# Kernel optimization log

Hardware: AMD Instinct MI355X
Metric: run time of the kernel (lower is better)

Reference implementation:

```python
import math
import jax, jax.numpy as jnp
import numpy as np

B, S, G, CMAX, T = 128, 256, 8, 6, 32
E, NH, L, Z = 64, 4, 2, 3
DFF = 4 * E


def _conv1d(x, w, b, pad):
    # x: [N, C, T], w: [O, I, K] -> [N, O, T]
    y = jax.lax.conv_general_dilated(x, w, (1,), [(pad, pad)], dimension_numbers=('NCH', 'OIH', 'NCH'))
    return y + b[None, :, None]


def _layernorm(x, g, b, eps=1e-5):
    m = jnp.mean(x, -1, keepdims=True)
    v = jnp.mean((x - m) ** 2, -1, keepdims=True)
    return (x - m) * jax.lax.rsqrt(v + eps) * g + b


def _pos_encoding(seq_len, dim):
    pos = jnp.arange(seq_len, dtype=jnp.float32)[:, None]
    div = jnp.exp(jnp.arange(0, dim, 2, dtype=jnp.float32) * (-math.log(10000.0) / dim))
    pe = jnp.zeros((seq_len, dim), dtype=jnp.float32)
    pe = pe.at[:, 0::2].set(jnp.sin(pos * div)).at[:, 1::2].set(jnp.cos(pos * div))
    return pe


def setup_inputs() -> dict:
    key = jax.random.key(0)
    ks = iter(jax.random.split(key, 48))
    def nrm(shape, s=0.05):
        return (jax.random.normal(next(ks), shape) * s).astype(jnp.float32)
    inp = {}
    inp['waveforms'] = jax.random.normal(next(ks), (B, S, CMAX, T), dtype=jnp.float32)
    inp['shank_ids'] = jax.random.randint(next(ks), (B, S), 0, G)
    lengths = jax.random.randint(next(ks), (B,), S // 2, S + 1)
    inp['mask'] = jnp.arange(S)[None, :] >= lengths[:, None]  # True = padded
    inp['conv1_w'] = nrm((G, 32, CMAX, 5), 0.1)
    inp['conv1_b'] = jnp.zeros((G, 32), jnp.float32)
    inp['conv2_w'] = nrm((G, E, 32, 3), 0.1)
    inp['conv2_b'] = jnp.zeros((G, E), jnp.float32)
    inp['shank_emb'] = nrm((G, E), 0.02)
    inp['in_proj_w'] = nrm((L, 3 * E, E))
    inp['in_proj_b'] = jnp.zeros((L, 3 * E), jnp.float32)
    inp['out_proj_w'] = nrm((L, E, E))
    inp['out_proj_b'] = jnp.zeros((L, E), jnp.float32)
    inp['ln1_g'] = jnp.ones((L, E), jnp.float32)
    inp['ln1_b'] = jnp.zeros((L, E), jnp.float32)
    inp['ff1_w'] = nrm((L, DFF, E))
    inp['ff1_b'] = jnp.zeros((L, DFF), jnp.float32)
    inp['ff2_w'] = nrm((L, E, DFF))
    inp['ff2_b'] = jnp.zeros((L, E), jnp.float32)
    inp['ln2_g'] = jnp.ones((L, E), jnp.float32)
    inp['ln2_b'] = jnp.zeros((L, E), jnp.float32)
    inp['cls_w1'] = nrm((E, E)); inp['cls_b1'] = jnp.zeros((E,), jnp.float32)
    inp['cls_w2'] = nrm((Z, E)); inp['cls_b2'] = jnp.zeros((Z,), jnp.float32)
    inp['mu_w1'] = nrm((Z, E, E)); inp['mu_b1'] = jnp.zeros((Z, E), jnp.float32)
    inp['mu_w2'] = nrm((Z, 2, E)); inp['mu_b2'] = jnp.zeros((Z, 2), jnp.float32)
    inp['ls_w1'] = nrm((Z, E, E)); inp['ls_b1'] = jnp.zeros((Z, E), jnp.float32)
    inp['ls_w2'] = nrm((Z, 2, E)); inp['ls_b2'] = jnp.zeros((Z, 2), jnp.float32)
    inp['d_w1'] = nrm((E, E)); inp['d_b1'] = jnp.zeros((E,), jnp.float32)
    inp['d_w2'] = nrm((1, E)); inp['d_b2'] = jnp.zeros((1,), jnp.float32)
    return inp


def reference(waveforms, shank_ids, mask, conv1_w, conv1_b, conv2_w, conv2_b, shank_emb,
              in_proj_w, in_proj_b, out_proj_w, out_proj_b, ln1_g, ln1_b,
              ff1_w, ff1_b, ff2_w, ff2_b, ln2_g, ln2_b,
              cls_w1, cls_b1, cls_w2, cls_b2, mu_w1, mu_b1, mu_w2, mu_b2,
              ls_w1, ls_b1, ls_w2, ls_b2, d_w1, d_b1, d_w2, d_b2):
    b, s, c, t = waveforms.shape
    e = shank_emb.shape[1]
    g = shank_emb.shape[0]
    x = waveforms.reshape(b * s, c, t)
    # per-shank conv encoders (MoE-style dispatch); loop over fixed small expert set
    embs = []
    for i in range(g):
        h1 = jax.nn.relu(_conv1d(x, conv1_w[i], conv1_b[i], 2))   # [N,32,T]
        h2 = jax.nn.relu(_conv1d(h1, conv2_w[i], conv2_b[i], 1))  # [N,E,T]
        embs.append(h2.mean(-1))                                  # AdaptiveAvgPool1d(1)
    emb_all = jnp.stack(embs, axis=1)                             # [N,G,E]
    sid = shank_ids.reshape(-1)
    emb = jnp.take_along_axis(emb_all, sid[:, None, None], axis=1)[:, 0]  # [N,E]
    active = (~mask).reshape(-1)
    emb = jnp.where(active[:, None], emb, 0.0).reshape(b, s, e)   # masked slots stay zero
    emb = emb + shank_emb[shank_ids] + _pos_encoding(s, e)[None]
    # post-norm transformer encoder, relu FFN, eval mode (dropout off)
    dh = e // NH
    key_bias = jnp.where(mask, -1e9, 0.0).astype(emb.dtype)[:, None, None, :]  # [B,1,1,S]
    h = emb
    for l in range(in_proj_w.shape[0]):
        qkv = h @ in_proj_w[l].T + in_proj_b[l]
        q, k, v = jnp.split(qkv, 3, axis=-1)
        q = q.reshape(b, s, NH, dh)
        k = k.reshape(b, s, NH, dh)
        v = v.reshape(b, s, NH, dh)
        scores = jnp.einsum('bqhd,bkhd->bhqk', q, k) / math.sqrt(dh) + key_bias
        attn = jax.nn.softmax(scores, axis=-1)
        o = jnp.einsum('bhqk,bkhd->bqhd', attn, v).reshape(b, s, e)
        o = o @ out_proj_w[l].T + out_proj_b[l]
        h = _layernorm(h + o, ln1_g[l], ln1_b[l])
        ff = jax.nn.relu(h @ ff1_w[l].T + ff1_b[l]) @ ff2_w[l].T + ff2_b[l]
        h = _layernorm(h + ff, ln2_g[l], ln2_b[l])
    am = active.reshape(b, s, 1).astype(h.dtype)
    pooled = (h * am).sum(1) / (am.sum(1) + 1e-8)                 # masked mean pool [B,E]
    cls_logits = jax.nn.relu(pooled @ cls_w1.T + cls_b1) @ cls_w2.T + cls_b2
    hz = jax.nn.relu(jnp.einsum('be,zfe->zbf', pooled, mu_w1) + mu_b1[:, None])
    mus = jnp.einsum('zbf,zof->bzo', hz, mu_w2) + mu_b2[None]     # [B,Z,2]
    hs = jax.nn.relu(jnp.einsum('be,zfe->zbf', pooled, ls_w1) + ls_b1[:, None])
    sigmas = jnp.exp(jnp.einsum('zbf,zof->bzo', hs, ls_w2) + ls_b2[None])  # [B,Z,2]
    d_pred = jax.nn.sigmoid(jax.nn.relu(pooled @ d_w1.T + d_b1) @ d_w2.T + d_b2)
    return jnp.concatenate([cls_logits, mus.reshape(b, -1), sigmas.reshape(b, -1), d_pred], axis=-1)
```

## Files before the change

### kernel.cpp

```cpp
#include <hip/hip_runtime.h>
#include <math.h>


typedef short bf16x8 __attribute__((ext_vector_type(8)));
typedef float f32x4 __attribute__((ext_vector_type(4)));

__device__ __forceinline__ unsigned short f2bf(float f) {
  unsigned u = __float_as_uint(f);
  u += 0x7fffu + ((u >> 16) & 1u);
  return (unsigned short)(u >> 16);
}

__device__ __forceinline__ bf16x8 ldfrag(const unsigned short* p) {
  return *reinterpret_cast<const bf16x8*>(p);
}

__device__ __forceinline__ bool is_masked(const void* mask_, int flag, int idx) {
  return flag ? (((const unsigned char*)mask_)[idx] != 0)
              : (((const int*)mask_)[idx] != 0);
}

__global__ void detect_mask_kernel(const unsigned int* __restrict__ mw,
                                   int* __restrict__ flag, int* __restrict__ counts,
                                   int* __restrict__ lens) {
  __shared__ int sh;
  if (threadIdx.x == 0) sh = 0;
  __syncthreads();
  int bad = 0;
  for (int i = threadIdx.x; i < 8192; i += 256)
    if (mw[i] > 1u) bad = 1;
  if (bad) atomicOr(&sh, 1);
  if (threadIdx.x < 8) counts[threadIdx.x] = 0;
  if (threadIdx.x < 128) lens[threadIdx.x] = 0;
  __syncthreads();
  if (threadIdx.x == 0) *flag = sh;
}

__global__ __launch_bounds__(256) void bin_kernel(
    const int* __restrict__ sid, const void* __restrict__ mask_,
    const int* __restrict__ flagp, int* __restrict__ counts,
    int* __restrict__ lens, int* __restrict__ idxbuf) {
  __shared__ int lcnt[8];
  __shared__ int lbase[8];
  int b = blockIdx.x, tid = threadIdx.x;
  int n = b * 256 + tid;
  int flag = *flagp;
  bool act = !is_masked(mask_, flag, n);
  int g = act ? sid[n] : 0;
  if (tid < 8) lcnt[tid] = 0;
  __syncthreads();
  int pos = 0;
  if (act) pos = atomicAdd(&lcnt[g], 1);
  __syncthreads();
  if (tid < 8) lbase[tid] = atomicAdd(&counts[tid], lcnt[tid]);
  if (tid == 0)
    lens[b] = lcnt[0] + lcnt[1] + lcnt[2] + lcnt[3] +
              lcnt[4] + lcnt[5] + lcnt[6] + lcnt[7];
  __syncthreads();
  if (act) idxbuf[g * 32768 + lbase[g] + pos] = n;
}

__global__ __launch_bounds__(256) void init_emb_kernel(
    const int* __restrict__ sid, const float* __restrict__ shank_emb,
    float* __restrict__ hout) {
  int i = blockIdx.x * 256 + threadIdx.x;
  int n = i >> 6, e = i & 63, s = n & 255;
  int g = sid[n];
  float div = __expf(-(float)(e & ~1) * (9.21034037f / 64.f));
  float angle = (float)s * div;
  float pe = (e & 1) ? cosf(angle) : sinf(angle);
  hout[i] = shank_emb[g * 64 + e] + pe;
}

__global__ __launch_bounds__(256) void conv_mfma_kernel(
    const int* __restrict__ idxbuf, const int* __restrict__ counts,
    const float* __restrict__ wav,
    const float* __restrict__ w1_, const float* __restrict__ b1_,
    const float* __restrict__ w2_, const float* __restrict__ b2_,
    const float* __restrict__ shank_emb, float* __restrict__ hout) {
  __shared__ __align__(16) unsigned short w1f[5][32][8];
  __shared__ __align__(16) unsigned short w2f[3][64][40];
  __shared__ float b1s[32];
  __shared__ float b2s[64];
  __shared__ __align__(16) unsigned short xw[4][36][8];
  __shared__ __align__(16) unsigned short h1w[4][34][40];
  int g = blockIdx.x & 7, bib = blockIdx.x >> 3;
  int tid = threadIdx.x;
  int wvx = tid >> 6, lane = tid & 63, quad = lane >> 4, l15 = lane & 15;
  for (int i = tid; i < 1280; i += 256) {
    int k = i >> 8, rest = i & 255, oc = rest >> 3, ic = rest & 7;
    w1f[k][oc][ic] = (ic < 6) ? f2bf(w1_[g * 960 + oc * 30 + ic * 5 + k]) : 0;
  }
  for (int i = tid; i < 7680; i += 256) {
    int k = i / 2560, rest = i % 2560, e = rest / 40, ic = rest % 40;
    w2f[k][e][ic] = (ic < 32) ? f2bf(w2_[g * 6144 + e * 96 + ic * 3 + k]) : 0;
  }
  if (tid < 32) b1s[tid] = b1_[g * 32 + tid];
  if (tid < 64) b2s[tid] = b2_[g * 64 + tid];
  {
    unsigned int* xz = (unsigned int*)&xw[wvx][0][0];
    for (int i = lane; i < 144; i += 64) xz[i] = 0;
    unsigned int* hz0 = (unsigned int*)&h1w[wvx][0][0];
    unsigned int* hz1 = (unsigned int*)&h1w[wvx][33][0];
    if (lane < 20) hz0[lane] = 0;
    else if (lane < 40) hz1[lane - 20] = 0;
  }
  __syncthreads();
  bf16x8 zf = {0, 0, 0, 0, 0, 0, 0, 0};
  bf16x8 bf1[2], bf1k4[2], bf2[3][4];
#pragma unroll
  for (int nt = 0; nt < 2; nt++) {
    bf1[nt] = ldfrag(&w1f[quad][nt * 16 + l15][0]);
    bf1k4[nt] = (quad == 0) ? ldfrag(&w1f[4][nt * 16 + l15][0]) : zf;
  }
#pragma unroll
  for (int k = 0; k < 3; k++)
#pragma unroll
    for (int nt = 0; nt < 4; nt++)
      bf2[k][nt] = ldfrag(&w2f[k][nt * 16 + l15][quad * 8]);
  float b1v0 = b1s[l15], b1v1 = b1s[16 + l15];
  float shank = shank_emb[g * 64 + lane];
  float dive = __expf(-(float)(lane & ~1) * (9.21034037f / 64.f));
  int cnt = counts[g];
  int wvg = bib * 4 + wvx;
  int ic_w = lane >> 3, t0_w = (lane & 7) * 4;
  for (int ti = wvg; ti < cnt; ti += 512) {
    int n = idxbuf[g * 32768 + ti];
    float4 v = make_float4(0.f, 0.f, 0.f, 0.f);
    if (lane < 48) v = *(const float4*)&wav[n * 192 + lane * 4];
    if (lane < 48) {
      xw[wvx][t0_w + 2][ic_w] = f2bf(v.x);
      xw[wvx][t0_w + 3][ic_w] = f2bf(v.y);
      xw[wvx][t0_w + 4][ic_w] = f2bf(v.z);
      xw[wvx][t0_w + 5][ic_w] = f2bf(v.w);
    }
    f32x4 c1[2][2];
#pragma unroll
    for (int mt = 0; mt < 2; mt++) {
      c1[mt][0] = (f32x4){b1v0, b1v0, b1v0, b1v0};
      c1[mt][1] = (f32x4){b1v1, b1v1, b1v1, b1v1};
    }
#pragma unroll
    for (int mt = 0; mt < 2; mt++) {
      bf16x8 afm = ldfrag(&xw[wvx][mt * 16 + l15 + quad][0]);
      bf16x8 af4 = (quad == 0) ? ldfrag(&xw[wvx][mt * 16 + l15 + 4][0]) : zf;
#pragma unroll
      for (int nt = 0; nt < 2; nt++) {
        c1[mt][nt] = __builtin_amdgcn_mfma_f32_16x16x32_bf16(afm, bf1[nt], c1[mt][nt], 0, 0, 0);
        c1[mt][nt] = __builtin_amdgcn_mfma_f32_16x16x32_bf16(af4, bf1k4[nt], c1[mt][nt], 0, 0, 0);
      }
    }
#pragma unroll
    for (int mt = 0; mt < 2; mt++)
#pragma unroll
      for (int nt = 0; nt < 2; nt++)
#pragma unroll
        for (int r = 0; r < 4; r++) {
          int t = mt * 16 + quad * 4 + r;
          h1w[wvx][t + 1][nt * 16 + l15] = f2bf(fmaxf(c1[mt][nt][r], 0.f));
        }
    f32x4 c2[2][4];
#pragma unroll
    for (int mt = 0; mt < 2; mt++)
#pragma unroll
      for (int nt = 0; nt < 4; nt++) {
        float bv = b2s[nt * 16 + l15];
        c2[mt][nt] = (f32x4){bv, bv, bv, bv};
      }
#pragma unroll
    for (int k = 0; k < 3; k++)
#pragma unroll
      for (int mt = 0; mt < 2; mt++) {
        bf16x8 af = ldfrag(&h1w[wvx][mt * 16 + l15 + k][quad * 8]);
#pragma unroll
        for (int nt = 0; nt < 4; nt++)
          c2[mt][nt] = __builtin_amdgcn_mfma_f32_16x16x32_bf16(af, bf2[k][nt], c2[mt][nt], 0, 0, 0);
      }
    float sums[4];
#pragma unroll
    for (int nt = 0; nt < 4; nt++) {
      float s = 0.f;
#pragma unroll
      for (int mt = 0; mt < 2; mt++)
#pragma unroll
        for (int r = 0; r < 4; r++) s += fmaxf(c2[mt][nt][r], 0.f);
      s += __shfl_xor(s, 16);
      s += __shfl_xor(s, 32);
      sums[nt] = s;
    }
    float t0 = __shfl(sums[0], l15);
    float t1 = __shfl(sums[1], l15);
    float t2 = __shfl(sums[2], l15);
    float t3 = __shfl(sums[3], l15);
    float val = (quad == 0) ? t0 : (quad == 1) ? t1 : (quad == 2) ? t2 : t3;
    float angle = (float)(n & 255) * dive;
    float pe = (lane & 1) ? cosf(angle) : sinf(angle);
    hout[(size_t)n * 64 + lane] = val * (1.f / 32.f) + shank + pe;
  }
}

__global__ __launch_bounds__(256) void attn_fused_kernel(
    const float* __restrict__ H, const float* __restrict__ Wqkv,
    const float* __restrict__ bqkv, const int* __restrict__ lens,
    float* __restrict__ o) {
  __shared__ __align__(16) unsigned short un[18432];
  __shared__ __align__(16) unsigned short wqs[16][72];
  __shared__ __align__(16) unsigned short wks[16][72];
  __shared__ __align__(16) unsigned short wvs[16][72];
  __shared__ __align__(16) unsigned short qs[256][24];
  __shared__ __align__(16) unsigned short kst[256][24];
  __shared__ __align__(16) unsigned short vT[16][264];
  __shared__ float bqs[16], bks[16], bvs[16];
  unsigned short (*hs)[72] = (unsigned short(*)[72])un;
  unsigned short (*pw)[16][264] = (unsigned short(*)[16][264])un;
  int bh = blockIdx.x;
  int b_ = bh >> 2, hd = bh & 3;
  int tid = threadIdx.x;
  int wvx = tid >> 6, lane = tid & 63, quad = lane >> 4, l15 = lane & 15;
  int len = lens[b_];
  const float* hb = H + (size_t)b_ * 256 * 64;
  for (int i = tid; i < 4096; i += 256) {
    int r = i >> 4, c4 = (i & 15) << 2;
    float4 v = *(const float4*)&hb[r * 64 + c4];
    short4 t;
    t.x = (short)f2bf(v.x); t.y = (short)f2bf(v.y);
    t.z = (short)f2bf(v.z); t.w = (short)f2bf(v.w);
    *(short4*)&hs[r][c4] = t;
  }
  for (int i = tid; i < 768; i += 256) {
    int r = i >> 4, c4 = (i & 15) << 2;
    int which = r >> 4, rr = r & 15;
    float4 v = *(const float4*)&Wqkv[(size_t)(which * 64 + hd * 16 + rr) * 64 + c4];
    float sc = (which == 0) ? 0.25f : 1.f;
    short4 t;
    t.x = (short)f2bf(v.x * sc); t.y = (short)f2bf(v.y * sc);
    t.z = (short)f2bf(v.z * sc); t.w = (short)f2bf(v.w * sc);
    unsigned short (*dst)[72] = (which == 0) ? wqs : (which == 1) ? wks : wvs;
    *(short4*)&dst[rr][c4] = t;
  }
  if (tid < 16) {
    bqs[tid] = 0.25f * bqkv[hd * 16 + tid];
    bks[tid] = bqkv[64 + hd * 16 + tid];
    bvs[tid] = bqkv[128 + hd * 16 + tid];
  }
  __syncthreads();
#pragma unroll
  for (int t4 = 0; t4 < 4; t4++) {
    int tile = wvx * 4 + t4;
    float bq = bqs[l15], bk = bks[l15];
    f32x4 aq = (f32x4){bq, bq, bq, bq};
    f32x4 ak = (f32x4){bk, bk, bk, bk};
    f32x4 av = (f32x4){bvs[quad * 4 + 0], bvs[quad * 4 + 1],
                       bvs[quad * 4 + 2], bvs[quad * 4 + 3]};
#pragma unroll
    for (int ks = 0; ks < 64; ks += 32) {
      bf16x8 af = ldfrag(&hs[tile * 16 + l15][ks + quad * 8]);
      aq = __builtin_amdgcn_mfma_f32_16x16x32_bf16(af, ldfrag(&wqs[l15][ks + quad * 8]), aq, 0, 0, 0);
      ak = __builtin_amdgcn_mfma_f32_16x16x32_bf16(af, ldfrag(&wks[l15][ks + quad * 8]), ak, 0, 0, 0);
      av = __builtin_amdgcn_mfma_f32_16x16x32_bf16(ldfrag(&wvs[l15][ks + quad * 8]), af, av, 0, 0, 0);
    }
#pragma unroll
    for (int r = 0; r < 4; r++) {
      qs[tile * 16 + quad * 4 + r][l15] = f2bf(aq[r]);
      kst[tile * 16 + quad * 4 + r][l15] = f2bf(ak[r]);
      vT[quad * 4 + r][tile * 16 + l15] = f2bf(av[r]);
    }
  }
  __syncthreads();
  bf16x8 zf = {0, 0, 0, 0, 0, 0, 0, 0};
  f32x4 zero = {0.f, 0.f, 0.f, 0.f};
#pragma unroll 1
  for (int j = 0; j < 4; j++) {
    int qt = wvx * 4 + j;
    bf16x8 bq = (quad < 2) ? ldfrag(&qs[qt * 16 + l15][quad * 8]) : zf;
    f32x4 s[16];
#pragma unroll
    for (int t = 0; t < 16; t++) {
      bf16x8 ak = (quad < 2) ? ldfrag(&kst[t * 16 + l15][quad * 8]) : zf;
      s[t] = __builtin_amdgcn_mfma_f32_16x16x32_bf16(ak, bq, zero, 0, 0, 0);
    }
    float mx = -1e30f;
#pragma unroll
    for (int t = 0; t < 16; t++)
#pragma unroll
      for (int r = 0; r < 4; r++) {
        int key = t * 16 + quad * 4 + r;
        float v = (key < len) ? s[t][r] : -1e30f;
        s[t][r] = v;
        mx = fmaxf(mx, v);
      }
    mx = fmaxf(mx, __shfl_xor(mx, 16));
    mx = fmaxf(mx, __shfl_xor(mx, 32));
    float sum = 0.f;
#pragma unroll
    for (int t = 0; t < 16; t++)
#pragma unroll
      for (int r = 0; r < 4; r++) {
        float p = __expf(s[t][r] - mx);
        s[t][r] = p;
        sum += p;
      }
    sum += __shfl_xor(sum, 16);
    sum += __shfl_xor(sum, 32);
#pragma unroll
    for (int t = 0; t < 16; t++) {
      short4 pp;
      pp.x = (short)f2bf(s[t][0]); pp.y = (short)f2bf(s[t][1]);
      pp.z = (short)f2bf(s[t][2]); pp.w = (short)f2bf(s[t][3]);
      *(short4*)&pw[wvx][l15][t * 16 + quad * 4] = pp;
    }
    f32x4 acc = zero;
#pragma unroll
    for (int c = 0; c < 8; c++) {
      bf16x8 avv = ldfrag(&vT[l15][c * 32 + quad * 8]);
      bf16x8 bp = ldfrag(&pw[wvx][l15][c * 32 + quad * 8]);
      acc = __builtin_amdgcn_mfma_f32_16x16x32_bf16(avv, bp, acc, 0, 0, 0);
    }
    float inv = 1.f / sum;
    float4 w;
    w.x = acc[0] * inv; w.y = acc[1] * inv;
    w.z = acc[2] * inv; w.w = acc[3] * inv;
    *(float4*)&o[(size_t)(b_ * 256 + qt * 16 + l15) * 64 + hd * 16 + quad * 4] = w;
  }
}

__global__ __launch_bounds__(256) void fused_rl_kernel(
    const float* __restrict__ obuf, float* __restrict__ H,
    const float* __restrict__ Wout, const float* __restrict__ bout,
    const float* __restrict__ ln1g, const float* __restrict__ ln1b,
    const float* __restrict__ Wff1, const float* __restrict__ bff1,
    const float* __restrict__ Wff2, const float* __restrict__ bff2,
    const float* __restrict__ ln2g, const float* __restrict__ ln2b) {
  __shared__ __align__(16) unsigned short Ao[64][72];
  __shared__ __align__(16) unsigned short Wo[64][72];
  __shared__ __align__(16) unsigned short W1s[256][72];
  __shared__ __align__(16) unsigned short W2s[64][264];
  __shared__ __align__(16) unsigned short h1b[64][72];
  __shared__ __align__(16) unsigned short ffa[64][264];
  __shared__ float h1f[64][68];
  int m0 = blockIdx.x * 64;
  int tid = threadIdx.x;
  int wvx = tid >> 6, lane = tid & 63, quad = lane >> 4, l15 = lane & 15;
  for (int i = tid; i < 1024; i += 256) {
    int r = i >> 4, c4 = (i & 15) << 2;
    float4 av = *(const float4*)&obuf[(size_t)(m0 + r) * 64 + c4];
    short4 t;
    t.x = (short)f2bf(av.x); t.y = (short)f2bf(av.y);
    t.z = (short)f2bf(av.z); t.w = (short)f2bf(av.w);
    *(short4*)&Ao[r][c4] = t;
    float4 wv4 = *(const float4*)&Wout[(size_t)r * 64 + c4];
    short4 u;
    u.x = (short)f2bf(wv4.x); u.y = (short)f2bf(wv4.y);
    u.z = (short)f2bf(wv4.z); u.w = (short)f2bf(wv4.w);
    *(short4*)&Wo[r][c4] = u;
  }
  for (int i = tid; i < 4096; i += 256) {
    int r = i >> 4, c4 = (i & 15) << 2;
    float4 wv4 = *(const float4*)&Wff1[(size_t)r * 64 + c4];
    short4 u;
    u.x = (short)f2bf(wv4.x); u.y = (short)f2bf(wv4.y);
    u.z = (short)f2bf(wv4.z); u.w = (short)f2bf(wv4.w);
    *(short4*)&W1s[r][c4] = u;
  }
  for (int i = tid; i < 4096; i += 256) {
    int r = i >> 6, c4 = (i & 63) << 2;
    float4 wv4 = *(const float4*)&Wff2[(size_t)r * 256 + c4];
    short4 u;
    u.x = (short)f2bf(wv4.x); u.y = (short)f2bf(wv4.y);
    u.z = (short)f2bf(wv4.z); u.w = (short)f2bf(wv4.w);
    *(short4*)&W2s[r][c4] = u;
  }
  __syncthreads();
  int lr = wvx * 16 + quad * 4;
  f32x4 acc[4];
#pragma unroll
  for (int nt = 0; nt < 4; nt++) {
    float b = bout[nt * 16 + l15];
    acc[nt] = (f32x4){b, b, b, b};
  }
#pragma unroll
  for (int ks = 0; ks < 64; ks += 32) {
    bf16x8 af = ldfrag(&Ao[wvx * 16 + l15][ks + quad * 8]);
#pragma unroll
    for (int nt = 0; nt < 4; nt++) {
      bf16x8 bfr = ldfrag(&Wo[nt * 16 + l15][ks + quad * 8]);
      acc[nt] = __builtin_amdgcn_mfma_f32_16x16x32_bf16(af, bfr, acc[nt], 0, 0, 0);
    }
  }
#pragma unroll
  for (int r = 0; r < 4; r++) {
    float rv[4];
    float s = 0.f;
#pragma unroll
    for (int nt = 0; nt < 4; nt++) {
      float v = acc[nt][r] + H[(size_t)(m0 + lr + r) * 64 + nt * 16 + l15];
      rv[nt] = v; s += v;
    }
    s += __shfl_xor(s, 1); s += __shfl_xor(s, 2);
    s += __shfl_xor(s, 4); s += __shfl_xor(s, 8);
    float mean = s * (1.f / 64.f);
    float vsum = 0.f;
#pragma unroll
    for (int nt = 0; nt < 4; nt++) { rv[nt] -= mean; vsum += rv[nt] * rv[nt]; }
    vsum += __shfl_xor(vsum, 1); vsum += __shfl_xor(vsum, 2);
    vsum += __shfl_xor(vsum, 4); vsum += __shfl_xor(vsum, 8);
    float inv = rsqrtf(vsum * (1.f / 64.f) + 1e-5f);
#pragma unroll
    for (int nt = 0; nt < 4; nt++) {
      int col = nt * 16 + l15;
      float hv = rv[nt] * inv * ln1g[col] + ln1b[col];
      h1f[lr + r][col] = hv;
      h1b[lr + r][col] = f2bf(hv);
    }
  }
  f32x4 a2[16];
#pragma unroll
  for (int nt = 0; nt < 16; nt++) {
    float b = bff1[nt * 16 + l15];
    a2[nt] = (f32x4){b, b, b, b};
  }
#pragma unroll
  for (int ks = 0; ks < 64; ks += 32) {
    bf16x8 af = ldfrag(&h1b[wvx * 16 + l15][ks + quad * 8]);
#pragma unroll
    for (int nt = 0; nt < 16; nt++) {
      bf16x8 bfr = ldfrag(&W1s[nt * 16 + l15][ks + quad * 8]);
      a2[nt] = __builtin_amdgcn_mfma_f32_16x16x32_bf16(af, bfr, a2[nt], 0, 0, 0);
    }
  }
#pragma unroll
  for (int nt = 0; nt < 16; nt++)
#pragma unroll
    for (int r = 0; r < 4; r++)
      ffa[lr + r][nt * 16 + l15] = f2bf(fmaxf(a2[nt][r], 0.f));
#pragma unroll
  for (int nt = 0; nt < 4; nt++) {
    float b = bff2[nt * 16 + l15];
    acc[nt] = (f32x4){b, b, b, b};
  }
#pragma unroll
  for (int ks = 0; ks < 256; ks += 32) {
    bf16x8 af = ldfrag(&ffa[wvx * 16 + l15][ks + quad * 8]);
#pragma unroll
    for (int nt = 0; nt < 4; nt++) {
      bf16x8 bfr = ldfrag(&W2s[nt * 16 + l15][ks + quad * 8]);
      acc[nt] = __builtin_amdgcn_mfma_f32_16x16x32_bf16(af, bfr, acc[nt], 0, 0, 0);
    }
  }
#pragma unroll
  for (int r = 0; r < 4; r++) {
    float rv[4];
    float s = 0.f;
#pragma unroll
    for (int nt = 0; nt < 4; nt++) {
      float v = acc[nt][r] + h1f[lr + r][nt * 16 + l15];
      rv[nt] = v; s += v;
    }
    s += __shfl_xor(s, 1); s += __shfl_xor(s, 2);
    s += __shfl_xor(s, 4); s += __shfl_xor(s, 8);
    float mean = s * (1.f / 64.f);
    float vsum = 0.f;
#pragma unroll
    for (int nt = 0; nt < 4; nt++) { rv[nt] -= mean; vsum += rv[nt] * rv[nt]; }
    vsum += __shfl_xor(vsum, 1); vsum += __shfl_xor(vsum, 2);
    vsum += __shfl_xor(vsum, 4); vsum += __shfl_xor(vsum, 8);
    float inv = rsqrtf(vsum * (1.f / 64.f) + 1e-5f);
#pragma unroll
    for (int nt = 0; nt < 4; nt++) {
      int col = nt * 16 + l15;
      H[(size_t)(m0 + lr + r) * 64 + col] = rv[nt] * inv * ln2g[col] + ln2b[col];
    }
  }
}

__global__ __launch_bounds__(256) void pool_heads_kernel(
    const float* __restrict__ h, const int* __restrict__ lens,
    const float* __restrict__ cls_w1, const float* __restrict__ cls_b1,
    const float* __restrict__ cls_w2, const float* __restrict__ cls_b2,
    const float* __restrict__ mu_w1, const float* __restrict__ mu_b1,
    const float* __restrict__ mu_w2, const float* __restrict__ mu_b2,
    const float* __restrict__ ls_w1, const float* __restrict__ ls_b1,
    const float* __restrict__ ls_w2, const float* __restrict__ ls_b2,
    const float* __restrict__ d_w1, const float* __restrict__ d_b1,
    const float* __restrict__ d_w2, const float* __restrict__ d_b2,
    float* __restrict__ out) {
  __shared__ float ps[4][64];
  __shared__ float p[64];
  __shared__ float t1[64];
  int b = blockIdx.x, tid = threadIdx.x;
  int e = tid & 63, sp = tid >> 6;
  int len = lens[b];
  {
    float sum = 0.f;
    int send = min(sp * 64 + 64, len);
    for (int s = sp * 64; s < send; s++) sum += h[(size_t)(b * 256 + s) * 64 + e];
    ps[sp][e] = sum;
  }
  __syncthreads();
  if (sp == 0)
    p[e] = (ps[0][e] + ps[1][e] + ps[2][e] + ps[3][e]) / ((float)len + 1e-8f);
  __syncthreads();
  if (tid < 64) {
    float a = cls_b1[tid];
    for (int j = 0; j < 64; j++) a += p[j] * cls_w1[tid * 64 + j];
    t1[tid] = fmaxf(a, 0.f);
  }
  __syncthreads();
  if (tid < 3) {
    float a2 = cls_b2[tid];
    for (int j = 0; j < 64; j++) a2 += t1[j] * cls_w2[tid * 64 + j];
    out[b * 16 + tid] = a2;
  }
  for (int z = 0; z < 3; z++) {
    __syncthreads();
    if (tid < 64) {
      float a = mu_b1[z * 64 + tid];
      for (int j = 0; j < 64; j++) a += p[j] * mu_w1[(z * 64 + tid) * 64 + j];
      t1[tid] = fmaxf(a, 0.f);
    }
    __syncthreads();
    if (tid < 2) {
      float a2 = mu_b2[z * 2 + tid];
      for (int j = 0; j < 64; j++) a2 += t1[j] * mu_w2[(z * 2 + tid) * 64 + j];
      out[b * 16 + 3 + z * 2 + tid] = a2;
    }
    __syncthreads();
    if (tid < 64) {
      float a = ls_b1[z * 64 + tid];
      for (int j = 0; j < 64; j++) a += p[j] * ls_w1[(z * 64 + tid) * 64 + j];
      t1[tid] = fmaxf(a, 0.f);
    }
    __syncthreads();
    if (tid < 2) {
      float a2 = ls_b2[z * 2 + tid];
      for (int j = 0; j < 64; j++) a2 += t1[j] * ls_w2[(z * 2 + tid) * 64 + j];
      out[b * 16 + 9 + z * 2 + tid] = __expf(a2);
    }
  }
  __syncthreads();
  if (tid < 64) {
    float a = d_b1[tid];
    for (int j = 0; j < 64; j++) a += p[j] * d_w1[tid * 64 + j];
    t1[tid] = fmaxf(a, 0.f);
  }
  __syncthreads();
  if (tid == 0) {
    float a2 = d_b2[0];
    for (int j = 0; j < 64; j++) a2 += t1[j] * d_w2[j];
    out[b * 16 + 15] = 1.f / (1.f + __expf(-a2));
  }
}

extern "C" void kernel_launch(void* const* d_in, const int* in_sizes, int n_in,
                              void* d_out, int out_size, void* d_ws, size_t ws_size,
                              hipStream_t stream) {
  const float* wav       = (const float*)d_in[0];
  const int*   sid       = (const int*)d_in[1];
  const void*  mask      = d_in[2];
  const float* conv1_w   = (const float*)d_in[3];
  const float* conv1_b   = (const float*)d_in[4];
  const float* conv2_w   = (const float*)d_in[5];
  const float* conv2_b   = (const float*)d_in[6];
  const float* shank_emb = (const float*)d_in[7];
  const float* in_proj_w = (const float*)d_in[8];
  const float* in_proj_b = (const float*)d_in[9];
  const float* out_proj_w= (const float*)d_in[10];
  const float* out_proj_b= (const float*)d_in[11];
  const float* ln1_g     = (const float*)d_in[12];
  const float* ln1_b     = (const float*)d_in[13];
  const float* ff1_w     = (const float*)d_in[14];
  const float* ff1_b     = (const float*)d_in[15];
  const float* ff2_w     = (const float*)d_in[16];
  const float* ff2_b     = (const float*)d_in[17];
  const float* ln2_g     = (const float*)d_in[18];
  const float* ln2_b     = (const float*)d_in[19];
  const float* cls_w1    = (const float*)d_in[20];
  const float* cls_b1    = (const float*)d_in[21];
  const float* cls_w2    = (const float*)d_in[22];
  const float* cls_b2    = (const float*)d_in[23];
  const float* mu_w1     = (const float*)d_in[24];
  const float* mu_b1     = (const float*)d_in[25];
  const float* mu_w2     = (const float*)d_in[26];
  const float* mu_b2     = (const float*)d_in[27];
  const float* ls_w1     = (const float*)d_in[28];
  const float* ls_b1     = (const float*)d_in[29];
  const float* ls_w2     = (const float*)d_in[30];
  const float* ls_b2     = (const float*)d_in[31];
  const float* d_w1      = (const float*)d_in[32];
  const float* d_b1      = (const float*)d_in[33];
  const float* d_w2      = (const float*)d_in[34];
  const float* d_b2      = (const float*)d_in[35];
  float* out = (float*)d_out;

  float* ws = (float*)d_ws;
  float* h      = ws;
  float* obuf   = ws + 2097152;
  int*   ip     = (int*)(ws + 10493952);
  int*   flag   = ip;
  int*   counts = ip + 8;
  int*   lens   = ip + 16;
  int*   idxbuf = ip + 144;

  detect_mask_kernel<<<1, 256, 0, stream>>>((const unsigned int*)mask, flag, counts, lens);
  bin_kernel<<<128, 256, 0, stream>>>(sid, mask, flag, counts, lens, idxbuf);
  init_emb_kernel<<<8192, 256, 0, stream>>>(sid, shank_emb, h);
  conv_mfma_kernel<<<1024, 256, 0, stream>>>(idxbuf, counts, wav, conv1_w, conv1_b,
                                             conv2_w, conv2_b, shank_emb, h);
  for (int l = 0; l < 2; l++) {
    attn_fused_kernel<<<512, 256, 0, stream>>>(h, in_proj_w + l * 12288,
                                               in_proj_b + l * 192, lens, obuf);
    fused_rl_kernel<<<512, 256, 0, stream>>>(
        obuf, h, out_proj_w + l * 4096, out_proj_b + l * 64,
        ln1_g + l * 64, ln1_b + l * 64,
        ff1_w + l * 16384, ff1_b + l * 256,
        ff2_w + l * 16384, ff2_b + l * 64,
        ln2_g + l * 64, ln2_b + l * 64);
  }
  pool_heads_kernel<<<128, 256, 0, stream>>>(h, lens, cls_w1, cls_b1, cls_w2, cls_b2,
                                             mu_w1, mu_b1, mu_w2, mu_b2,
                                             ls_w1, ls_b1, ls_w2, ls_b2,
                                             d_w1, d_b1, d_w2, d_b2, out);
}
```

Before: 321.9 us.

## Pre-convert weights and activations to bf16 once and read MFMA fragments from global

```diff
diff --git a/kernel.cpp b/kernel.cpp
--- a/kernel.cpp
+++ b/kernel.cpp
@@ -18,6 +18,36 @@
 __device__ __forceinline__ bool is_masked(const void* mask_, int flag, int idx) {
   return flag ? (((const unsigned char*)mask_)[idx] != 0)
               : (((const int*)mask_)[idx] != 0);
+}
+
+__global__ __launch_bounds__(256) void prep_weights_kernel(
+    const float* __restrict__ in_proj_w, const float* __restrict__ out_proj_w,
+    const float* __restrict__ ff1_w, const float* __restrict__ ff2_w,
+    const float* __restrict__ w1_, const float* __restrict__ w2_,
+    unsigned short* __restrict__ wb) {
+  int i = blockIdx.x * 256 + threadIdx.x;
+  if (i < 24576) {
+    int rem = i % 12288, row = rem / 64;
+    float v = in_proj_w[i];
+    if (row < 64) v *= 0.25f;
+    wb[i] = f2bf(v);
+  } else if (i < 32768) {
+    wb[i] = f2bf(out_proj_w[i - 24576]);
+  } else if (i < 65536) {
+    wb[i] = f2bf(ff1_w[i - 32768]);
+  } else if (i < 98304) {
+    wb[i] = f2bf(ff2_w[i - 65536]);
+  } else if (i < 108544) {
+    int j = i - 98304;
+    int g = j / 1280, rem = j % 1280;
+    int k = rem >> 8, rest = rem & 255, oc = rest >> 3, ic = rest & 7;
+    wb[i] = (ic < 6) ? f2bf(w1_[g * 960 + oc * 30 + ic * 5 + k]) : 0;
+  } else if (i < 169984) {
+    int j = i - 108544;
+    int g = j / 7680, rem = j % 7680;
+    int k = rem / 2560, rest = rem % 2560, e = rest / 40, ic = rest % 40;
+    wb[i] = (ic < 32) ? f2bf(w2_[g * 6144 + e * 96 + ic * 3 + k]) : 0;
+  }
 }
 
 __global__ void detect_mask_kernel(const unsigned int* __restrict__ mw,
@@ -62,22 +92,24 @@
 
 __global__ __launch_bounds__(256) void init_emb_kernel(
     const int* __restrict__ sid, const float* __restrict__ shank_emb,
-    float* __restrict__ hout) {
+    float* __restrict__ hout, unsigned short* __restrict__ hb) {
   int i = blockIdx.x * 256 + threadIdx.x;
   int n = i >> 6, e = i & 63, s = n & 255;
   int g = sid[n];
   float div = __expf(-(float)(e & ~1) * (9.21034037f / 64.f));
   float angle = (float)s * div;
   float pe = (e & 1) ? cosf(angle) : sinf(angle);
-  hout[i] = shank_emb[g * 64 + e] + pe;
+  float v = shank_emb[g * 64 + e] + pe;
+  hout[i] = v;
+  hb[i] = f2bf(v);
 }
 
 __global__ __launch_bounds__(256) void conv_mfma_kernel(
     const int* __restrict__ idxbuf, const int* __restrict__ counts,
-    const float* __restrict__ wav,
-    const float* __restrict__ w1_, const float* __restrict__ b1_,
-    const float* __restrict__ w2_, const float* __restrict__ b2_,
-    const float* __restrict__ shank_emb, float* __restrict__ hout) {
+    const float* __restrict__ wav, const unsigned short* __restrict__ wb,
+    const float* __restrict__ b1_, const float* __restrict__ b2_,
+    const float* __restrict__ shank_emb, float* __restrict__ hout,
+    unsigned short* __restrict__ hb) {
   __shared__ __align__(16) unsigned short w1f[5][32][8];
   __shared__ __align__(16) unsigned short w2f[3][64][40];
   __shared__ float b1s[32];
@@ -87,13 +119,13 @@
   int g = blockIdx.x & 7, bib = blockIdx.x >> 3;
   int tid = threadIdx.x;
   int wvx = tid >> 6, lane = tid & 63, quad = lane >> 4, l15 = lane & 15;
-  for (int i = tid; i < 1280; i += 256) {
-    int k = i >> 8, rest = i & 255, oc = rest >> 3, ic = rest & 7;
-    w1f[k][oc][ic] = (ic < 6) ? f2bf(w1_[g * 960 + oc * 30 + ic * 5 + k]) : 0;
-  }
-  for (int i = tid; i < 7680; i += 256) {
-    int k = i / 2560, rest = i % 2560, e = rest / 40, ic = rest % 40;
-    w2f[k][e][ic] = (ic < 32) ? f2bf(w2_[g * 6144 + e * 96 + ic * 3 + k]) : 0;
+  {
+    const uint4* s1 = (const uint4*)(wb + 98304 + g * 1280);
+    uint4* d1 = (uint4*)&w1f[0][0][0];
+    for (int i = tid; i < 160; i += 256) d1[i] = s1[i];
+    const uint4* s2 = (const uint4*)(wb + 108544 + g * 7680);
+    uint4* d2 = (uint4*)&w2f[0][0][0];
+    for (int i = tid; i < 960; i += 256) d2[i] = s2[i];
   }
   if (tid < 32) b1s[tid] = b1_[g * 32 + tid];
   if (tid < 64) b2s[tid] = b2_[g * 64 + tid];
@@ -124,7 +156,7 @@
   int cnt = counts[g];
   int wvg = bib * 4 + wvx;
   int ic_w = lane >> 3, t0_w = (lane & 7) * 4;
-  for (int ti = wvg; ti < cnt; ti += 512) {
+  for (int ti = wvg; ti < cnt; ti += 640) {
     int n = idxbuf[g * 32768 + ti];
     float4 v = make_float4(0.f, 0.f, 0.f, 0.f);
     if (lane < 48) v = *(const float4*)&wav[n * 192 + lane * 4];
@@ -195,69 +227,46 @@
     float val = (quad == 0) ? t0 : (quad == 1) ? t1 : (quad == 2) ? t2 : t3;
     float angle = (float)(n & 255) * dive;
     float pe = (lane & 1) ? cosf(angle) : sinf(angle);
-    hout[(size_t)n * 64 + lane] = val * (1.f / 32.f) + shank + pe;
+    float hv = val * (1.f / 32.f) + shank + pe;
+    hout[(size_t)n * 64 + lane] = hv;
+    hb[(size_t)n * 64 + lane] = f2bf(hv);
   }
 }
 
 __global__ __launch_bounds__(256) void attn_fused_kernel(
-    const float* __restrict__ H, const float* __restrict__ Wqkv,
+    const unsigned short* __restrict__ hb, const unsigned short* __restrict__ wqkv,
     const float* __restrict__ bqkv, const int* __restrict__ lens,
-    float* __restrict__ o) {
-  __shared__ __align__(16) unsigned short un[18432];
-  __shared__ __align__(16) unsigned short wqs[16][72];
-  __shared__ __align__(16) unsigned short wks[16][72];
-  __shared__ __align__(16) unsigned short wvs[16][72];
+    unsigned short* __restrict__ obuf) {
   __shared__ __align__(16) unsigned short qs[256][24];
   __shared__ __align__(16) unsigned short kst[256][24];
   __shared__ __align__(16) unsigned short vT[16][264];
-  __shared__ float bqs[16], bks[16], bvs[16];
-  unsigned short (*hs)[72] = (unsigned short(*)[72])un;
-  unsigned short (*pw)[16][264] = (unsigned short(*)[16][264])un;
+  __shared__ __align__(16) unsigned short pw[4][16][264];
   int bh = blockIdx.x;
   int b_ = bh >> 2, hd = bh & 3;
   int tid = threadIdx.x;
   int wvx = tid >> 6, lane = tid & 63, quad = lane >> 4, l15 = lane & 15;
   int len = lens[b_];
-  const float* hb = H + (size_t)b_ * 256 * 64;
-  for (int i = tid; i < 4096; i += 256) {
-    int r = i >> 4, c4 = (i & 15) << 2;
-    float4 v = *(const float4*)&hb[r * 64 + c4];
-    short4 t;
-    t.x = (short)f2bf(v.x); t.y = (short)f2bf(v.y);
-    t.z = (short)f2bf(v.z); t.w = (short)f2bf(v.w);
-    *(short4*)&hs[r][c4] = t;
-  }
-  for (int i = tid; i < 768; i += 256) {
-    int r = i >> 4, c4 = (i & 15) << 2;
-    int which = r >> 4, rr = r & 15;
-    float4 v = *(const float4*)&Wqkv[(size_t)(which * 64 + hd * 16 + rr) * 64 + c4];
-    float sc = (which == 0) ? 0.25f : 1.f;
-    short4 t;
-    t.x = (short)f2bf(v.x * sc); t.y = (short)f2bf(v.y * sc);
-    t.z = (short)f2bf(v.z * sc); t.w = (short)f2bf(v.w * sc);
-    unsigned short (*dst)[72] = (which == 0) ? wqs : (which == 1) ? wks : wvs;
-    *(short4*)&dst[rr][c4] = t;
-  }
-  if (tid < 16) {
-    bqs[tid] = 0.25f * bqkv[hd * 16 + tid];
-    bks[tid] = bqkv[64 + hd * 16 + tid];
-    bvs[tid] = bqkv[128 + hd * 16 + tid];
-  }
-  __syncthreads();
+  const unsigned short* hbb = hb + (size_t)b_ * 256 * 64;
+  const unsigned short* wq = wqkv + (hd * 16) * 64;
+  const unsigned short* wk = wqkv + (64 + hd * 16) * 64;
+  const unsigned short* wv = wqkv + (128 + hd * 16) * 64;
+  float bq_ = 0.25f * bqkv[hd * 16 + l15];
+  float bk_ = bqkv[64 + hd * 16 + l15];
+  f32x4 bv_;
+#pragma unroll
+  for (int r = 0; r < 4; r++) bv_[r] = bqkv[128 + hd * 16 + quad * 4 + r];
 #pragma unroll
   for (int t4 = 0; t4 < 4; t4++) {
     int tile = wvx * 4 + t4;
-    float bq = bqs[l15], bk = bks[l15];
-    f32x4 aq = (f32x4){bq, bq, bq, bq};
-    f32x4 ak = (f32x4){bk, bk, bk, bk};
-    f32x4 av = (f32x4){bvs[quad * 4 + 0], bvs[quad * 4 + 1],
-                       bvs[quad * 4 + 2], bvs[quad * 4 + 3]};
+    f32x4 aq = (f32x4){bq_, bq_, bq_, bq_};
+    f32x4 ak = (f32x4){bk_, bk_, bk_, bk_};
+    f32x4 av = bv_;
 #pragma unroll
     for (int ks = 0; ks < 64; ks += 32) {
-      bf16x8 af = ldfrag(&hs[tile * 16 + l15][ks + quad * 8]);
-      aq = __builtin_amdgcn_mfma_f32_16x16x32_bf16(af, ldfrag(&wqs[l15][ks + quad * 8]), aq, 0, 0, 0);
-      ak = __builtin_amdgcn_mfma_f32_16x16x32_bf16(af, ldfrag(&wks[l15][ks + quad * 8]), ak, 0, 0, 0);
-      av = __builtin_amdgcn_mfma_f32_16x16x32_bf16(ldfrag(&wvs[l15][ks + quad * 8]), af, av, 0, 0, 0);
+      bf16x8 af = ldfrag(hbb + (tile * 16 + l15) * 64 + ks + quad * 8);
+      aq = __builtin_amdgcn_mfma_f32_16x16x32_bf16(af, ldfrag(wq + l15 * 64 + ks + quad * 8), aq, 0, 0, 0);
+      ak = __builtin_amdgcn_mfma_f32_16x16x32_bf16(af, ldfrag(wk + l15 * 64 + ks + quad * 8), ak, 0, 0, 0);
+      av = __builtin_amdgcn_mfma_f32_16x16x32_bf16(ldfrag(wv + l15 * 64 + ks + quad * 8), af, av, 0, 0, 0);
     }
 #pragma unroll
     for (int r = 0; r < 4; r++) {
@@ -317,60 +326,26 @@
       acc = __builtin_amdgcn_mfma_f32_16x16x32_bf16(avv, bp, acc, 0, 0, 0);
     }
     float inv = 1.f / sum;
-    float4 w;
-    w.x = acc[0] * inv; w.y = acc[1] * inv;
-    w.z = acc[2] * inv; w.w = acc[3] * inv;
-    *(float4*)&o[(size_t)(b_ * 256 + qt * 16 + l15) * 64 + hd * 16 + quad * 4] = w;
+    short4 w;
+    w.x = (short)f2bf(acc[0] * inv); w.y = (short)f2bf(acc[1] * inv);
+    w.z = (short)f2bf(acc[2] * inv); w.w = (short)f2bf(acc[3] * inv);
+    *(short4*)&obuf[(size_t)(b_ * 256 + qt * 16 + l15) * 64 + hd * 16 + quad * 4] = w;
   }
 }
 
 __global__ __launch_bounds__(256) void fused_rl_kernel(
-    const float* __restrict__ obuf, float* __restrict__ H,
-    const float* __restrict__ Wout, const float* __restrict__ bout,
+    const unsigned short* __restrict__ obuf, float* __restrict__ H,
+    unsigned short* __restrict__ Hb,
+    const unsigned short* __restrict__ wout, const float* __restrict__ bout,
     const float* __restrict__ ln1g, const float* __restrict__ ln1b,
-    const float* __restrict__ Wff1, const float* __restrict__ bff1,
-    const float* __restrict__ Wff2, const float* __restrict__ bff2,
+    const unsigned short* __restrict__ wff1, const float* __restrict__ bff1,
+    const unsigned short* __restrict__ wff2, const float* __restrict__ bff2,
     const float* __restrict__ ln2g, const float* __restrict__ ln2b) {
-  __shared__ __align__(16) unsigned short Ao[64][72];
-  __shared__ __align__(16) unsigned short Wo[64][72];
-  __shared__ __align__(16) unsigned short W1s[256][72];
-  __shared__ __align__(16) unsigned short W2s[64][264];
   __shared__ __align__(16) unsigned short h1b[64][72];
   __shared__ __align__(16) unsigned short ffa[64][264];
-  __shared__ float h1f[64][68];
   int m0 = blockIdx.x * 64;
   int tid = threadIdx.x;
   int wvx = tid >> 6, lane = tid & 63, quad = lane >> 4, l15 = lane & 15;
-  for (int i = tid; i < 1024; i += 256) {
-    int r = i >> 4, c4 = (i & 15) << 2;
-    float4 av = *(const float4*)&obuf[(size_t)(m0 + r) * 64 + c4];
-    short4 t;
-    t.x = (short)f2bf(av.x); t.y = (short)f2bf(av.y);
-    t.z = (short)f2bf(av.z); t.w = (short)f2bf(av.w);
-    *(short4*)&Ao[r][c4] = t;
-    float4 wv4 = *(const float4*)&Wout[(size_t)r * 64 + c4];
-    short4 u;
-    u.x = (short)f2bf(wv4.x); u.y = (short)f2bf(wv4.y);
-    u.z = (short)f2bf(wv4.z); u.w = (short)f2bf(wv4.w);
-    *(short4*)&Wo[r][c4] = u;
-  }
-  for (int i = tid; i < 4096; i += 256) {
-    int r = i >> 4, c4 = (i & 15) << 2;
-    float4 wv4 = *(const float4*)&Wff1[(size_t)r * 64 + c4];
-    short4 u;
-    u.x = (short)f2bf(wv4.x); u.y = (short)f2bf(wv4.y);
-    u.z = (short)f2bf(wv4.z); u.w = (short)f2bf(wv4.w);
-    *(short4*)&W1s[r][c4] = u;
-  }
-  for (int i = tid; i < 4096; i += 256) {
-    int r = i >> 6, c4 = (i & 63) << 2;
-    float4 wv4 = *(const float4*)&Wff2[(size_t)r * 256 + c4];
-    short4 u;
-    u.x = (short)f2bf(wv4.x); u.y = (short)f2bf(wv4.y);
-    u.z = (short)f2bf(wv4.z); u.w = (short)f2bf(wv4.w);
-    *(short4*)&W2s[r][c4] = u;
-  }
-  __syncthreads();
   int lr = wvx * 16 + quad * 4;
   f32x4 acc[4];
 #pragma unroll
@@ -380,13 +355,14 @@
   }
 #pragma unroll
   for (int ks = 0; ks < 64; ks += 32) {
-    bf16x8 af = ldfrag(&Ao[wvx * 16 + l15][ks + quad * 8]);
+    bf16x8 af = ldfrag(obuf + (size_t)(m0 + wvx * 16 + l15) * 64 + ks + quad * 8);
 #pragma unroll
     for (int nt = 0; nt < 4; nt++) {
-      bf16x8 bfr = ldfrag(&Wo[nt * 16 + l15][ks + quad * 8]);
+      bf16x8 bfr = ldfrag(wout + (nt * 16 + l15) * 64 + ks + quad * 8);
       acc[nt] = __builtin_amdgcn_mfma_f32_16x16x32_bf16(af, bfr, acc[nt], 0, 0, 0);
     }
   }
+  float h1reg[4][4];
 #pragma unroll
   for (int r = 0; r < 4; r++) {
     float rv[4];
@@ -409,7 +385,7 @@
     for (int nt = 0; nt < 4; nt++) {
       int col = nt * 16 + l15;
       float hv = rv[nt] * inv * ln1g[col] + ln1b[col];
-      h1f[lr + r][col] = hv;
+      h1reg[r][nt] = hv;
       h1b[lr + r][col] = f2bf(hv);
     }
   }
@@ -424,7 +400,7 @@
     bf16x8 af = ldfrag(&h1b[wvx * 16 + l15][ks + quad * 8]);
 #pragma unroll
     for (int nt = 0; nt < 16; nt++) {
-      bf16x8 bfr = ldfrag(&W1s[nt * 16 + l15][ks + quad * 8]);
+      bf16x8 bfr = ldfrag(wff1 + (nt * 16 + l15) * 64 + ks + quad * 8);
       a2[nt] = __builtin_amdgcn_mfma_f32_16x16x32_bf16(af, bfr, a2[nt], 0, 0, 0);
     }
   }
@@ -443,7 +419,7 @@
     bf16x8 af = ldfrag(&ffa[wvx * 16 + l15][ks + quad * 8]);
 #pragma unroll
     for (int nt = 0; nt < 4; nt++) {
-      bf16x8 bfr = ldfrag(&W2s[nt * 16 + l15][ks + quad * 8]);
+      bf16x8 bfr = ldfrag(wff2 + (nt * 16 + l15) * 256 + ks + quad * 8);
       acc[nt] = __builtin_amdgcn_mfma_f32_16x16x32_bf16(af, bfr, acc[nt], 0, 0, 0);
     }
   }
@@ -453,7 +429,7 @@
     float s = 0.f;
 #pragma unroll
     for (int nt = 0; nt < 4; nt++) {
-      float v = acc[nt][r] + h1f[lr + r][nt * 16 + l15];
+      float v = acc[nt][r] + h1reg[r][nt];
       rv[nt] = v; s += v;
     }
     s += __shfl_xor(s, 1); s += __shfl_xor(s, 2);
@@ -468,7 +444,9 @@
 #pragma unroll
     for (int nt = 0; nt < 4; nt++) {
       int col = nt * 16 + l15;
-      H[(size_t)(m0 + lr + r) * 64 + col] = rv[nt] * inv * ln2g[col] + ln2b[col];
+      float hv = rv[nt] * inv * ln2g[col] + ln2b[col];
+      H[(size_t)(m0 + lr + r) * 64 + col] = hv;
+      Hb[(size_t)(m0 + lr + r) * 64 + col] = f2bf(hv);
     }
   }
 }
@@ -593,27 +571,32 @@
   float* out = (float*)d_out;
 
   float* ws = (float*)d_ws;
-  float* h      = ws;
-  float* obuf   = ws + 2097152;
+  float*          h     = ws;
+  unsigned short* hb    = (unsigned short*)(ws + 2097152);
+  unsigned short* obufb = (unsigned short*)(ws + 3145728);
+  unsigned short* wb    = (unsigned short*)(ws + 4194304);
   int*   ip     = (int*)(ws + 10493952);
   int*   flag   = ip;
   int*   counts = ip + 8;
   int*   lens   = ip + 16;
   int*   idxbuf = ip + 144;
 
+  prep_weights_kernel<<<664, 256, 0, stream>>>(in_proj_w, out_proj_w, ff1_w, ff2_w,
+                                               conv1_w, conv2_w, wb);
   detect_mask_kernel<<<1, 256, 0, stream>>>((const unsigned int*)mask, flag, counts, lens);
   bin_kernel<<<128, 256, 0, stream>>>(sid, mask, flag, counts, lens, idxbuf);
-  init_emb_kernel<<<8192, 256, 0, stream>>>(sid, shank_emb, h);
-  conv_mfma_kernel<<<1024, 256, 0, stream>>>(idxbuf, counts, wav, conv1_w, conv1_b,
-                                             conv2_w, conv2_b, shank_emb, h);
+  init_emb_kernel<<<8192, 256, 0, stream>>>(sid, shank_emb, h, hb);
+  conv_mfma_kernel<<<1280, 256, 0, stream>>>(idxbuf, counts, wav, wb, conv1_b, conv2_b,
+                                             shank_emb, h, hb);
   for (int l = 0; l < 2; l++) {
-    attn_fused_kernel<<<512, 256, 0, stream>>>(h, in_proj_w + l * 12288,
-                                               in_proj_b + l * 192, lens, obuf);
+    attn_fused_kernel<<<512, 256, 0, stream>>>(hb, wb + l * 12288,
+                                               in_proj_b + l * 192, lens, obufb);
     fused_rl_kernel<<<512, 256, 0, stream>>>(
-        obuf, h, out_proj_w + l * 4096, out_proj_b + l * 64,
+        obufb, h, hb,
+        wb + 24576 + l * 4096, out_proj_b + l * 64,
         ln1_g + l * 64, ln1_b + l * 64,
-        ff1_w + l * 16384, ff1_b + l * 256,
-        ff2_w + l * 16384, ff2_b + l * 64,
+        wb + 32768 + l * 16384, ff1_b + l * 256,
+        wb + 65536 + l * 16384, ff2_b + l * 64,
         ln2_g + l * 64, ln2_b + l * 64);
   }
   pool_heads_kernel<<<128, 256, 0, stream>>>(h, lens, cls_w1, cls_b1, cls_w2, cls_b2,
```

After: 308.0 us. -4.3%, faster.
